# Kernel tuning notes

Measured on AMD Instinct MI355X. Metric: run time of the kernel, lower is better.

The kernel has to match this reference:

```python
import jax, jax.numpy as jnp
import numpy as np

NUM_HEADS = 4
GROUPS = 8
EPS = 1e-5

def setup_inputs() -> dict:
    key = jax.random.key(0)
    ks = jax.random.split(key, 4)
    C = 256
    x = jax.random.normal(ks[0], (4, C, 64, 64), dtype=jnp.float32)
    qkv_w = jax.random.normal(ks[1], (3 * C, C), dtype=jnp.float32) * (C ** -0.5)
    qkv_b = jnp.zeros((3 * C,), dtype=jnp.float32)
    proj_w = jax.random.normal(ks[2], (C, C), dtype=jnp.float32) * (C ** -0.5)
    proj_b = jnp.zeros((C,), dtype=jnp.float32)
    gamma = jnp.ones((C,), dtype=jnp.float32)
    beta = jnp.zeros((C,), dtype=jnp.float32)
    return {"x": x, "qkv_w": qkv_w, "qkv_b": qkv_b, "proj_w": proj_w, "proj_b": proj_b, "gamma": gamma, "beta": beta}

def group_norm(x, gamma, beta):
    B, C, H, W = x.shape
    xg = x.reshape(B, GROUPS, C // GROUPS, H, W)
    mean = xg.mean(axis=(2, 3, 4), keepdims=True)
    var = xg.var(axis=(2, 3, 4), keepdims=True)
    xn = (xg - mean) * jax.lax.rsqrt(var + EPS)
    xn = xn.reshape(B, C, H, W)
    return xn * gamma[None, :, None, None] + beta[None, :, None, None]

def reference(x, qkv_w, qkv_b, proj_w, proj_b, gamma, beta):
    B, C, H, W = x.shape
    L = H * W
    hd = C // NUM_HEADS
    xn = group_norm(x, gamma, beta)  # (B,C,H,W)
    xf = xn.reshape(B, C, L)  # tokens along last axis
    # 1x1 conv == per-pixel linear: (3C, C) @ (B, C, L)
    qkv = jnp.einsum('oc,bcl->bol', qkv_w, xf) + qkv_b[None, :, None]
    q, k, v = jnp.split(qkv, 3, axis=1)  # each (B,C,L)
    q = q.reshape(B, NUM_HEADS, hd, L)
    k = k.reshape(B, NUM_HEADS, hd, L)
    v = v.reshape(B, NUM_HEADS, hd, L)
    scale = hd ** -0.5
    attn = jnp.einsum('bhdq,bhdk->bhqk', q, k) * scale
    attn = jax.nn.softmax(attn, axis=-1)
    out = jnp.einsum('bhqk,bhdk->bhdq', attn, v)  # (B,h,hd,L)
    out = out.reshape(B, C, L)
    out = jnp.einsum('oc,bcl->bol', proj_w, out) + proj_b[None, :, None]
    return out.reshape(B, C, H, W) + xn
```

## Files before the change

kernel.cpp:

```cpp
#include <hip/hip_runtime.h>
#include <math.h>

#define L 4096
#define LOG2E_O8 0.18033688011112042f

typedef float f32x16 __attribute__((ext_vector_type(16)));
typedef __bf16 bf16x8 __attribute__((ext_vector_type(8)));

static __device__ __forceinline__ float fast_exp2(float x) {
    return __builtin_amdgcn_exp2f(x);
}
static __device__ __forceinline__ unsigned short f2bfu(float f) {
    unsigned int u = __builtin_bit_cast(unsigned int, f);
    u += 0x7fffu + ((u >> 16) & 1u);
    return (unsigned short)(u >> 16);
}
static __device__ __forceinline__ unsigned int cvtpk(float a, float b) {
    unsigned int r;
    asm("v_cvt_pk_bf16_f32 %0, %1, %2" : "=v"(r) : "v"(a), "v"(b));
    return r;
}
static __device__ __forceinline__ void pl32swap(unsigned int& a, unsigned int& b) {
    auto r = __builtin_amdgcn_permlane32_swap(a, b, false, false);
    a = r[0];
    b = r[1];
}
static __device__ __forceinline__ bf16x8 ld_frag_g(const unsigned short* p) {
    uint4 v = *(const uint4*)p;
    return __builtin_bit_cast(bf16x8, v);
}
static __device__ __forceinline__ bf16x8 ld_frag_s(const unsigned short* p) {
    uint4 v = *(const uint4*)p;
    return __builtin_bit_cast(bf16x8, v);
}

__global__ __launch_bounds__(256) void gn_stats_part_kernel(const float* __restrict__ x,
                                                            float2* __restrict__ part) {
    const int blk = blockIdx.x;
    const float4* p = (const float4*)(x + (size_t)blk * 8192);
    float sum = 0.f, sq = 0.f;
    for (int i = threadIdx.x; i < 2048; i += 256) {
        float4 v = p[i];
        sum += (v.x + v.y) + (v.z + v.w);
        sq  += (v.x * v.x + v.y * v.y) + (v.z * v.z + v.w * v.w);
    }
#pragma unroll
    for (int off = 1; off < 64; off <<= 1) {
        sum += __shfl_xor(sum, off);
        sq  += __shfl_xor(sq, off);
    }
    __shared__ float red[8];
    const int t = threadIdx.x;
    if ((t & 63) == 0) { red[(t >> 6) * 2] = sum; red[(t >> 6) * 2 + 1] = sq; }
    __syncthreads();
    if (t == 0) {
        float s = red[0] + red[2] + red[4] + red[6];
        float q = red[1] + red[3] + red[5] + red[7];
        part[blk] = make_float2(s, q);
    }
}

__global__ __launch_bounds__(64) void gn_stats_final_kernel(const float2* __restrict__ part,
                                                            float2* __restrict__ stats) {
    const int bg = threadIdx.x;
    if (bg < 32) {
        float s = 0.f, q = 0.f;
#pragma unroll
        for (int i = 0; i < 16; ++i) {
            float2 v = part[bg * 16 + i];
            s += v.x; q += v.y;
        }
        const float inv_n = 1.0f / (32.0f * L);
        float mean = s * inv_n;
        float var = q * inv_n - mean * mean;
        stats[bg] = make_float2(mean, rsqrtf(var + 1e-5f));
    }
}

__global__ __launch_bounds__(256) void wcvt_kernel(const float* __restrict__ qkv_w,
                                                   const float* __restrict__ proj_w,
                                                   unsigned short* __restrict__ Wqb,
                                                   unsigned short* __restrict__ Wpb) {
    const int i4 = (blockIdx.x * 256 + threadIdx.x) * 4;
    const float* src;
    unsigned short* dst;
    if (i4 < 196608) { src = qkv_w + i4; dst = Wqb + i4; }
    else             { src = proj_w + (i4 - 196608); dst = Wpb + (i4 - 196608); }
    float4 v = *(const float4*)src;
    ushort4 o;
    o.x = f2bfu(v.x); o.y = f2bfu(v.y); o.z = f2bfu(v.z); o.w = f2bfu(v.w);
    *(ushort4*)dst = o;
}

__global__ __launch_bounds__(256) void gn_apply_kernel(const float* __restrict__ x,
                                                       const float* __restrict__ gamma,
                                                       const float* __restrict__ beta,
                                                       const float2* __restrict__ stats,
                                                       unsigned short* __restrict__ xnT) {
    __shared__ float tile[64][68];
    const int t = threadIdx.x;
    const int b = blockIdx.z, c0 = blockIdx.y * 64, l0 = blockIdx.x * 64;
    const int lc = (t & 15) * 4, cr = t >> 4;
#pragma unroll
    for (int p = 0; p < 4; ++p) {
        const int c = c0 + cr + p * 16;
        const float2 st = stats[b * 8 + (c >> 5)];
        const float g = gamma[c] * st.y;
        const float be = beta[c] - st.x * g;
        float4 v = *(const float4*)&x[((size_t)b * 256 + c) * L + l0 + lc];
        float4 o;
        o.x = v.x * g + be; o.y = v.y * g + be; o.z = v.z * g + be; o.w = v.w * g + be;
        *(float4*)&tile[cr + p * 16][lc] = o;
    }
    __syncthreads();
    const int lr = t >> 2, cc = (t & 3) * 16;
    unsigned short* dst = &xnT[((size_t)b * L + l0 + lr) * 256 + c0 + cc];
#pragma unroll
    for (int g4 = 0; g4 < 4; ++g4) {
        ushort4 o4;
        o4.x = f2bfu(tile[cc + g4 * 4 + 0][lr]);
        o4.y = f2bfu(tile[cc + g4 * 4 + 1][lr]);
        o4.z = f2bfu(tile[cc + g4 * 4 + 2][lr]);
        o4.w = f2bfu(tile[cc + g4 * 4 + 3][lr]);
        *(ushort4*)&dst[g4 * 4] = o4;
    }
}

__global__ __launch_bounds__(256) void qkv_gemm_kernel(
        const unsigned short* __restrict__ xnT,
        const unsigned short* __restrict__ Wq,
        const float* __restrict__ bias,
        unsigned short* __restrict__ Qb,
        unsigned short* __restrict__ Kb,
        unsigned short* __restrict__ Vb) {
    const int t = threadIdx.x, lane = t & 63, w = t >> 6;
    const int l5 = lane >> 5, l31 = lane & 31;
    const int wn = w & 1, wm = w >> 1;
    const int n0 = blockIdx.x * 128 + wn * 64;
    const int m0 = blockIdx.y * 128 + wm * 64;
    const int b = blockIdx.z;
    const unsigned short* ap = xnT + ((size_t)b * L + n0 + l31) * 256 + l5 * 8;
    const unsigned short* bp = Wq + (size_t)(m0 + l31) * 256 + l5 * 8;
    f32x16 acc[2][2];
#pragma unroll
    for (int i = 0; i < 2; ++i)
#pragma unroll
        for (int j = 0; j < 2; ++j)
#pragma unroll
            for (int r = 0; r < 16; ++r) acc[i][j][r] = 0.f;
#pragma unroll
    for (int k0 = 0; k0 < 256; k0 += 16) {
        bf16x8 a0 = ld_frag_g(ap + k0);
        bf16x8 a1 = ld_frag_g(ap + 32 * 256 + k0);
        bf16x8 b0 = ld_frag_g(bp + k0);
        bf16x8 b1 = ld_frag_g(bp + 32 * 256 + k0);
        acc[0][0] = __builtin_amdgcn_mfma_f32_32x32x16_bf16(a0, b0, acc[0][0], 0, 0, 0);
        acc[0][1] = __builtin_amdgcn_mfma_f32_32x32x16_bf16(a0, b1, acc[0][1], 0, 0, 0);
        acc[1][0] = __builtin_amdgcn_mfma_f32_32x32x16_bf16(a1, b0, acc[1][0], 0, 0, 0);
        acc[1][1] = __builtin_amdgcn_mfma_f32_32x32x16_bf16(a1, b1, acc[1][1], 0, 0, 0);
    }
    const int sec = m0 >> 8;
    const size_t bh = (size_t)(b * 4 + ((m0 >> 6) & 3));
#pragma unroll
    for (int j = 0; j < 2; ++j) {
        const int m = m0 + j * 32 + l31;
        const int d = m & 63;
        const float bi = bias[m];
        if (sec < 2) {
            unsigned short* dst = (sec ? Kb : Qb) + bh * L * 64 + d;
            const float sc = (sec == 0) ? LOG2E_O8 : 1.0f;
#pragma unroll
            for (int i = 0; i < 2; ++i)
#pragma unroll
                for (int r = 0; r < 16; ++r) {
                    const int n = n0 + i * 32 + (r & 3) + 8 * (r >> 2) + 4 * l5;
                    dst[(size_t)n * 64] = f2bfu((acc[i][j][r] + bi) * sc);
                }
        } else {
            unsigned short* dst = Vb + (bh * 64 + d) * L;
#pragma unroll
            for (int i = 0; i < 2; ++i)
#pragma unroll
                for (int g = 0; g < 4; ++g) {
                    const int n = n0 + i * 32 + 8 * g + 4 * l5;
                    ushort4 st;
                    st.x = f2bfu(acc[i][j][4 * g + 0] + bi);
                    st.y = f2bfu(acc[i][j][4 * g + 1] + bi);
                    st.z = f2bfu(acc[i][j][4 * g + 2] + bi);
                    st.w = f2bfu(acc[i][j][4 * g + 3] + bi);
                    *(ushort4*)&dst[n] = st;
                }
        }
    }
}

__global__ __launch_bounds__(256, 2) void attn_kernel(
        const unsigned short* __restrict__ Qb,
        const unsigned short* __restrict__ Kb,
        const unsigned short* __restrict__ Vb,
        unsigned short* __restrict__ aoT) {
    const int t = threadIdx.x;
    const int lane = t & 63, w = t >> 6;
    const int l5 = lane >> 5, l31 = lane & 31;
    const int n = blockIdx.x;
    const int bh_i = n & 15;
    const int qt = n >> 4;
    const int b = bh_i >> 2, h = bh_i & 3;
    const int q0 = qt * 128 + w * 32;
    const size_t bh = (size_t)bh_i;

    __shared__ alignas(16) unsigned short Kt[2][32][72];
    __shared__ alignas(16) unsigned short Vt[2][64][40];

    const unsigned short* qp = Qb + (bh * L + q0 + l31) * 64 + l5 * 8;
    bf16x8 qf[4];
#pragma unroll
    for (int dc = 0; dc < 4; ++dc) qf[dc] = ld_frag_g(qp + dc * 16);

    const int kr = t >> 3, kq = t & 7;
    const int vd = t >> 2, vp = t & 3;
    const unsigned short* kgsrc = Kb + bh * L * 64 + kr * 64 + kq * 8;
    const unsigned short* vgsrc = Vb + (bh * 64 + vd) * L + vp * 8;

    f32x16 o0, o1;
#pragma unroll
    for (int r = 0; r < 16; ++r) { o0[r] = 0.f; o1[r] = 0.f; }
    float4 ls = make_float4(0.f, 0.f, 0.f, 0.f);

    {
        uint4 kv = *(const uint4*)kgsrc;
        uint4 vv = *(const uint4*)vgsrc;
        *(uint4*)&Kt[0][kr][kq * 8] = kv;
        *(uint4*)&Vt[0][vd][vp * 8] = vv;
    }
    __syncthreads();

    for (int kc = 0; kc < 128; ++kc) {
        const int buf = kc & 1;
        uint4 knx, vnx;
        if (kc < 127) {
            knx = *(const uint4*)(kgsrc + (size_t)(kc + 1) * 2048);
            vnx = *(const uint4*)(vgsrc + (kc + 1) * 32);
        }
        bf16x8 kf[4], vf[2][2];
#pragma unroll
        for (int dc = 0; dc < 4; ++dc)
            kf[dc] = ld_frag_s(&Kt[buf][l31][dc * 16 + l5 * 8]);
#pragma unroll
        for (int dh = 0; dh < 2; ++dh)
#pragma unroll
            for (int h16 = 0; h16 < 2; ++h16)
                vf[dh][h16] = ld_frag_s(&Vt[buf][dh * 32 + l31][h16 * 16 + l5 * 8]);
        f32x16 s;
#pragma unroll
        for (int r = 0; r < 16; ++r) s[r] = 0.f;
#pragma unroll
        for (int dc = 0; dc < 4; ++dc)
            s = __builtin_amdgcn_mfma_f32_32x32x16_bf16(kf[dc], qf[dc], s, 0, 0, 0);
#pragma unroll
        for (int r = 0; r < 16; ++r) s[r] = fast_exp2(s[r]);
#pragma unroll
        for (int g = 0; g < 4; ++g) {
            ls.x += s[4 * g + 0];
            ls.y += s[4 * g + 1];
            ls.z += s[4 * g + 2];
            ls.w += s[4 * g + 3];
        }
        unsigned int w0 = cvtpk(s[0],  s[1]);
        unsigned int w1 = cvtpk(s[2],  s[3]);
        unsigned int w2 = cvtpk(s[4],  s[5]);
        unsigned int w3 = cvtpk(s[6],  s[7]);
        unsigned int w4 = cvtpk(s[8],  s[9]);
        unsigned int w5 = cvtpk(s[10], s[11]);
        unsigned int w6 = cvtpk(s[12], s[13]);
        unsigned int w7 = cvtpk(s[14], s[15]);
        pl32swap(w0, w2);
        pl32swap(w1, w3);
        pl32swap(w4, w6);
        pl32swap(w5, w7);
        int4 p0v, p1v;
        p0v.x = (int)w0; p0v.y = (int)w1; p0v.z = (int)w2; p0v.w = (int)w3;
        p1v.x = (int)w4; p1v.y = (int)w5; p1v.z = (int)w6; p1v.w = (int)w7;
        bf16x8 pb0 = __builtin_bit_cast(bf16x8, p0v);
        bf16x8 pb1 = __builtin_bit_cast(bf16x8, p1v);
        o0 = __builtin_amdgcn_mfma_f32_32x32x16_bf16(vf[0][0], pb0, o0, 0, 0, 0);
        o0 = __builtin_amdgcn_mfma_f32_32x32x16_bf16(vf[0][1], pb1, o0, 0, 0, 0);
        o1 = __builtin_amdgcn_mfma_f32_32x32x16_bf16(vf[1][0], pb0, o1, 0, 0, 0);
        o1 = __builtin_amdgcn_mfma_f32_32x32x16_bf16(vf[1][1], pb1, o1, 0, 0, 0);
        if (kc < 127) {
            *(uint4*)&Kt[buf ^ 1][kr][kq * 8] = knx;
            *(uint4*)&Vt[buf ^ 1][vd][vp * 8] = vnx;
        }
        __syncthreads();
    }
    float lrun = (ls.x + ls.y) + (ls.z + ls.w);
    lrun += __shfl_xor(lrun, 32);
    const float inv = 1.f / lrun;
    unsigned short* op = aoT + ((size_t)b * L + q0 + l31) * 256 + h * 64 + 4 * l5;
#pragma unroll
    for (int g = 0; g < 4; ++g) {
        uint2 st;
        st.x = cvtpk(o0[4 * g + 0] * inv, o0[4 * g + 1] * inv);
        st.y = cvtpk(o0[4 * g + 2] * inv, o0[4 * g + 3] * inv);
        *(uint2*)&op[8 * g] = st;
        uint2 st2;
        st2.x = cvtpk(o1[4 * g + 0] * inv, o1[4 * g + 1] * inv);
        st2.y = cvtpk(o1[4 * g + 2] * inv, o1[4 * g + 3] * inv);
        *(uint2*)&op[32 + 8 * g] = st2;
    }
}

__global__ __launch_bounds__(256) void proj_gemm_kernel(
        const unsigned short* __restrict__ aoT,
        const unsigned short* __restrict__ Wp,
        const float* __restrict__ bias,
        const float* __restrict__ x,
        const float* __restrict__ gamma,
        const float* __restrict__ beta,
        const float2* __restrict__ stats,
        float* __restrict__ out) {
    const int t = threadIdx.x, lane = t & 63, w = t >> 6;
    const int l5 = lane >> 5, l31 = lane & 31;
    const int wn = w & 1, wm = w >> 1;
    const int n0 = blockIdx.x * 64 + wn * 32;
    const int m0 = blockIdx.y * 128 + wm * 64;
    const int b = blockIdx.z;
    const unsigned short* ap = aoT + ((size_t)b * L + n0 + l31) * 256 + l5 * 8;
    const unsigned short* bp = Wp + (size_t)(m0 + l31) * 256 + l5 * 8;
    f32x16 acc[2];
#pragma unroll
    for (int j = 0; j < 2; ++j)
#pragma unroll
        for (int r = 0; r < 16; ++r) acc[j][r] = 0.f;
#pragma unroll
    for (int k0 = 0; k0 < 256; k0 += 16) {
        bf16x8 a  = ld_frag_g(ap + k0);
        bf16x8 b0 = ld_frag_g(bp + k0);
        bf16x8 b1 = ld_frag_g(bp + 32 * 256 + k0);
        acc[0] = __builtin_amdgcn_mfma_f32_32x32x16_bf16(a, b0, acc[0], 0, 0, 0);
        acc[1] = __builtin_amdgcn_mfma_f32_32x32x16_bf16(a, b1, acc[1], 0, 0, 0);
    }
#pragma unroll
    for (int j = 0; j < 2; ++j) {
        const int co = m0 + j * 32 + l31;
        const float2 st = stats[b * 8 + (co >> 5)];
        const float g = gamma[co] * st.y;
        const float be = beta[co] - st.x * g + bias[co];
        const float* xr = &x[((size_t)b * 256 + co) * L];
        float* orow = &out[((size_t)b * 256 + co) * L];
#pragma unroll
        for (int q = 0; q < 4; ++q) {
            const int n = n0 + 8 * q + 4 * l5;
            float4 xv = *(const float4*)&xr[n];
            float4 ov;
            ov.x = acc[j][4 * q + 0] + (xv.x * g + be);
            ov.y = acc[j][4 * q + 1] + (xv.y * g + be);
            ov.z = acc[j][4 * q + 2] + (xv.z * g + be);
            ov.w = acc[j][4 * q + 3] + (xv.w * g + be);
            *(float4*)&orow[n] = ov;
        }
    }
}

extern "C" void kernel_launch(void* const* d_in, const int* in_sizes, int n_in,
                              void* d_out, int out_size, void* d_ws, size_t ws_size,
                              hipStream_t stream) {
    const float* x      = (const float*)d_in[0];
    const float* qkv_w  = (const float*)d_in[1];
    const float* qkv_b  = (const float*)d_in[2];
    const float* proj_w = (const float*)d_in[3];
    const float* proj_b = (const float*)d_in[4];
    const float* gamma  = (const float*)d_in[5];
    const float* beta   = (const float*)d_in[6];
    float* out = (float*)d_out;

    char* ws = (char*)d_ws;
    float2* stats       = (float2*)ws;
    unsigned short* Wqb = (unsigned short*)(ws + 512);
    unsigned short* Wpb = (unsigned short*)(ws + 512 + 393216);
    unsigned short* xnT = (unsigned short*)(ws + 524800);
    unsigned short* Qb  = (unsigned short*)(ws + 524800 + 8388608);
    unsigned short* Kb  = Qb + (size_t)16 * L * 64;
    unsigned short* Vb  = Kb + (size_t)16 * L * 64;
    unsigned short* aoT = Vb + (size_t)16 * L * 64;
    float2* spart       = (float2*)(ws + 524800);

    gn_stats_part_kernel<<<dim3(512), dim3(256), 0, stream>>>(x, spart);
    gn_stats_final_kernel<<<dim3(1), dim3(64), 0, stream>>>(spart, stats);
    wcvt_kernel<<<dim3(256), dim3(256), 0, stream>>>(qkv_w, proj_w, Wqb, Wpb);
    gn_apply_kernel<<<dim3(64, 4, 4), dim3(256), 0, stream>>>(x, gamma, beta, stats, xnT);
    qkv_gemm_kernel<<<dim3(32, 6, 4), dim3(256), 0, stream>>>(xnT, Wqb, qkv_b, Qb, Kb, Vb);
    attn_kernel<<<dim3(512), dim3(256), 0, stream>>>(Qb, Kb, Vb, aoT);
    proj_gemm_kernel<<<dim3(64, 2, 4), dim3(256), 0, stream>>>(aoT, Wpb, proj_b, x, gamma, beta, stats, out);
}
```

Baseline: 226.0 us.

## Split attention over key halves and merge partial results in a separate kernel

The attention kernel now splits the 4096-key range into two halves, launching 1024 blocks instead of 512, and writes unnormalized fp32 partial outputs and row sums to workspace. A new merge kernel adds the two partials, normalizes, and writes the bf16 output used by the projection. Launch bounds rise to 4 blocks per CU so more waves can be resident. The cost is about 32 MB of extra fp32 traffic and one more launch. The merge relies on the softmax having no running max, so both halves share the same exponent base.

```diff
diff --git a/kernel.cpp b/kernel.cpp
--- a/kernel.cpp
+++ b/kernel.cpp
@@ -194,18 +194,20 @@
     }
 }
 
-__global__ __launch_bounds__(256, 2) void attn_kernel(
+__global__ __launch_bounds__(256, 4) void attn_kernel(
         const unsigned short* __restrict__ Qb,
         const unsigned short* __restrict__ Kb,
         const unsigned short* __restrict__ Vb,
-        unsigned short* __restrict__ aoT) {
+        float* __restrict__ Po,
+        float* __restrict__ Pl) {
     const int t = threadIdx.x;
     const int lane = t & 63, w = t >> 6;
     const int l5 = lane >> 5, l31 = lane & 31;
     const int n = blockIdx.x;
     const int bh_i = n & 15;
-    const int qt = n >> 4;
-    const int b = bh_i >> 2, h = bh_i & 3;
+    const int r = n >> 4;
+    const int qt = r & 31;
+    const int kh = r >> 5;
     const int q0 = qt * 128 + w * 32;
     const size_t bh = (size_t)bh_i;
 
@@ -219,12 +221,12 @@
 
     const int kr = t >> 3, kq = t & 7;
     const int vd = t >> 2, vp = t & 3;
-    const unsigned short* kgsrc = Kb + bh * L * 64 + kr * 64 + kq * 8;
-    const unsigned short* vgsrc = Vb + (bh * 64 + vd) * L + vp * 8;
+    const unsigned short* kgsrc = Kb + bh * L * 64 + (size_t)kh * 2048 * 64 + kr * 64 + kq * 8;
+    const unsigned short* vgsrc = Vb + (bh * 64 + vd) * L + kh * 2048 + vp * 8;
 
     f32x16 o0, o1;
 #pragma unroll
-    for (int r = 0; r < 16; ++r) { o0[r] = 0.f; o1[r] = 0.f; }
+    for (int r2 = 0; r2 < 16; ++r2) { o0[r2] = 0.f; o1[r2] = 0.f; }
     float4 ls = make_float4(0.f, 0.f, 0.f, 0.f);
 
     {
@@ -235,10 +237,10 @@
     }
     __syncthreads();
 
-    for (int kc = 0; kc < 128; ++kc) {
+    for (int kc = 0; kc < 64; ++kc) {
         const int buf = kc & 1;
         uint4 knx, vnx;
-        if (kc < 127) {
+        if (kc < 63) {
             knx = *(const uint4*)(kgsrc + (size_t)(kc + 1) * 2048);
             vnx = *(const uint4*)(vgsrc + (kc + 1) * 32);
         }
@@ -253,12 +255,12 @@
                 vf[dh][h16] = ld_frag_s(&Vt[buf][dh * 32 + l31][h16 * 16 + l5 * 8]);
         f32x16 s;
 #pragma unroll
-        for (int r = 0; r < 16; ++r) s[r] = 0.f;
+        for (int r2 = 0; r2 < 16; ++r2) s[r2] = 0.f;
 #pragma unroll
         for (int dc = 0; dc < 4; ++dc)
             s = __builtin_amdgcn_mfma_f32_32x32x16_bf16(kf[dc], qf[dc], s, 0, 0, 0);
 #pragma unroll
-        for (int r = 0; r < 16; ++r) s[r] = fast_exp2(s[r]);
+        for (int r2 = 0; r2 < 16; ++r2) s[r2] = fast_exp2(s[r2]);
 #pragma unroll
         for (int g = 0; g < 4; ++g) {
             ls.x += s[4 * g + 0];
@@ -287,7 +289,7 @@
         o0 = __builtin_amdgcn_mfma_f32_32x32x16_bf16(vf[0][1], pb1, o0, 0, 0, 0);
         o1 = __builtin_amdgcn_mfma_f32_32x32x16_bf16(vf[1][0], pb0, o1, 0, 0, 0);
         o1 = __builtin_amdgcn_mfma_f32_32x32x16_bf16(vf[1][1], pb1, o1, 0, 0, 0);
-        if (kc < 127) {
+        if (kc < 63) {
             *(uint4*)&Kt[buf ^ 1][kr][kq * 8] = knx;
             *(uint4*)&Vt[buf ^ 1][vd][vp * 8] = vnx;
         }
@@ -295,18 +297,43 @@
     }
     float lrun = (ls.x + ls.y) + (ls.z + ls.w);
     lrun += __shfl_xor(lrun, 32);
-    const float inv = 1.f / lrun;
-    unsigned short* op = aoT + ((size_t)b * L + q0 + l31) * 256 + h * 64 + 4 * l5;
+    float* pp = Po + ((size_t)(kh * 16 + bh_i) * 4096 + q0 + l31) * 64 + 4 * l5;
 #pragma unroll
     for (int g = 0; g < 4; ++g) {
-        uint2 st;
-        st.x = cvtpk(o0[4 * g + 0] * inv, o0[4 * g + 1] * inv);
-        st.y = cvtpk(o0[4 * g + 2] * inv, o0[4 * g + 3] * inv);
-        *(uint2*)&op[8 * g] = st;
-        uint2 st2;
-        st2.x = cvtpk(o1[4 * g + 0] * inv, o1[4 * g + 1] * inv);
-        st2.y = cvtpk(o1[4 * g + 2] * inv, o1[4 * g + 3] * inv);
-        *(uint2*)&op[32 + 8 * g] = st2;
+        *(float4*)&pp[8 * g] =
+            make_float4(o0[4 * g + 0], o0[4 * g + 1], o0[4 * g + 2], o0[4 * g + 3]);
+        *(float4*)&pp[32 + 8 * g] =
+            make_float4(o1[4 * g + 0], o1[4 * g + 1], o1[4 * g + 2], o1[4 * g + 3]);
+    }
+    if (l5 == 0) Pl[(size_t)(kh * 16 + bh_i) * 4096 + q0 + l31] = lrun;
+}
+
+__global__ __launch_bounds__(256) void attn_merge_kernel(
+        const float* __restrict__ Po,
+        const float* __restrict__ Pl,
+        unsigned short* __restrict__ aoT) {
+    const int t = threadIdx.x;
+    const int ri = blockIdx.x * 64 + (t >> 2);
+    const int d0 = (t & 3) * 16;
+    const int bh = ri >> 12, q = ri & 4095;
+    const int b = bh >> 2, h = bh & 3;
+    const float l0 = Pl[ri], l1 = Pl[65536 + ri];
+    const float inv = 1.f / (l0 + l1);
+    const float* p0 = Po + (size_t)ri * 64 + d0;
+    const float* p1 = p0 + (size_t)65536 * 64;
+    unsigned short* op = aoT + ((size_t)b * L + q) * 256 + h * 64 + d0;
+#pragma unroll
+    for (int g = 0; g < 2; ++g) {
+        float4 a0 = *(const float4*)&p0[g * 8 + 0];
+        float4 a1 = *(const float4*)&p0[g * 8 + 4];
+        float4 c0 = *(const float4*)&p1[g * 8 + 0];
+        float4 c1 = *(const float4*)&p1[g * 8 + 4];
+        uint4 st;
+        st.x = cvtpk((a0.x + c0.x) * inv, (a0.y + c0.y) * inv);
+        st.y = cvtpk((a0.z + c0.z) * inv, (a0.w + c0.w) * inv);
+        st.z = cvtpk((a1.x + c1.x) * inv, (a1.y + c1.y) * inv);
+        st.w = cvtpk((a1.z + c1.z) * inv, (a1.w + c1.w) * inv);
+        *(uint4*)&op[g * 8] = st;
     }
 }
 
@@ -383,6 +410,8 @@
     unsigned short* Kb  = Qb + (size_t)16 * L * 64;
     unsigned short* Vb  = Kb + (size_t)16 * L * 64;
     unsigned short* aoT = Vb + (size_t)16 * L * 64;
+    float* Po           = (float*)(ws + 42467840);
+    float* Pl           = (float*)(ws + 42467840 + 33554432);
     float2* spart       = (float2*)(ws + 524800);
 
     gn_stats_part_kernel<<<dim3(512), dim3(256), 0, stream>>>(x, spart);
@@ -390,6 +419,7 @@
     wcvt_kernel<<<dim3(256), dim3(256), 0, stream>>>(qkv_w, proj_w, Wqb, Wpb);
     gn_apply_kernel<<<dim3(64, 4, 4), dim3(256), 0, stream>>>(x, gamma, beta, stats, xnT);
     qkv_gemm_kernel<<<dim3(32, 6, 4), dim3(256), 0, stream>>>(xnT, Wqb, qkv_b, Qb, Kb, Vb);
-    attn_kernel<<<dim3(512), dim3(256), 0, stream>>>(Qb, Kb, Vb, aoT);
+    attn_kernel<<<dim3(1024), dim3(256), 0, stream>>>(Qb, Kb, Vb, Po, Pl);
+    attn_merge_kernel<<<dim3(1024), dim3(256), 0, stream>>>(Po, Pl, aoT);
     proj_gemm_kernel<<<dim3(64, 2, 4), dim3(256), 0, stream>>>(aoT, Wpb, proj_b, x, gamma, beta, stats, out);
 }
```

New measurement: 221.3 us. 2.1% less time.

## Double key tile per iteration and interleave two S tiles with MFMA priority

Applied to the files above, without the earlier changes.

The attention loop now processes 64 keys per iteration instead of 32, loading two K and V fragment sets and computing two score tiles, which halves the number of barriers and shared-memory staging steps. The exp/convert work of the second tile is interleaved after the first tile's PV MFMAs, and s_setprio raises wave priority around MFMA groups to encourage overlap of matrix and vector work across waves. The launch-bounds occupancy hint of 2 is dropped and shared memory grows, so register pressure and occupancy may change.

```diff
diff --git a/kernel.cpp b/kernel.cpp
--- a/kernel.cpp
+++ b/kernel.cpp
@@ -194,7 +194,7 @@
     }
 }
 
-__global__ __launch_bounds__(256, 2) void attn_kernel(
+__global__ __launch_bounds__(256) void attn_kernel(
         const unsigned short* __restrict__ Qb,
         const unsigned short* __restrict__ Kb,
         const unsigned short* __restrict__ Vb,
@@ -209,87 +209,139 @@
     const int q0 = qt * 128 + w * 32;
     const size_t bh = (size_t)bh_i;
 
-    __shared__ alignas(16) unsigned short Kt[2][32][72];
-    __shared__ alignas(16) unsigned short Vt[2][64][40];
+    __shared__ alignas(16) unsigned short Kt[2][64][72];
+    __shared__ alignas(16) unsigned short Vt[2][64][72];
 
     const unsigned short* qp = Qb + (bh * L + q0 + l31) * 64 + l5 * 8;
     bf16x8 qf[4];
 #pragma unroll
     for (int dc = 0; dc < 4; ++dc) qf[dc] = ld_frag_g(qp + dc * 16);
 
-    const int kr = t >> 3, kq = t & 7;
-    const int vd = t >> 2, vp = t & 3;
-    const unsigned short* kgsrc = Kb + bh * L * 64 + kr * 64 + kq * 8;
-    const unsigned short* vgsrc = Vb + (bh * 64 + vd) * L + vp * 8;
+    const int sr = t >> 2, sp = t & 3;
+    const unsigned short* kgsrc = Kb + bh * L * 64 + sr * 64 + sp * 16;
+    const unsigned short* vgsrc = Vb + (bh * 64 + sr) * L + sp * 16;
 
     f32x16 o0, o1;
 #pragma unroll
-    for (int r = 0; r < 16; ++r) { o0[r] = 0.f; o1[r] = 0.f; }
+    for (int r2 = 0; r2 < 16; ++r2) { o0[r2] = 0.f; o1[r2] = 0.f; }
     float4 ls = make_float4(0.f, 0.f, 0.f, 0.f);
 
     {
-        uint4 kv = *(const uint4*)kgsrc;
-        uint4 vv = *(const uint4*)vgsrc;
-        *(uint4*)&Kt[0][kr][kq * 8] = kv;
-        *(uint4*)&Vt[0][vd][vp * 8] = vv;
+        uint4 k0 = *(const uint4*)kgsrc;
+        uint4 k1 = *(const uint4*)(kgsrc + 8);
+        uint4 v0 = *(const uint4*)vgsrc;
+        uint4 v1 = *(const uint4*)(vgsrc + 8);
+        *(uint4*)&Kt[0][sr][sp * 16]     = k0;
+        *(uint4*)&Kt[0][sr][sp * 16 + 8] = k1;
+        *(uint4*)&Vt[0][sr][sp * 16]     = v0;
+        *(uint4*)&Vt[0][sr][sp * 16 + 8] = v1;
     }
     __syncthreads();
 
-    for (int kc = 0; kc < 128; ++kc) {
-        const int buf = kc & 1;
-        uint4 knx, vnx;
-        if (kc < 127) {
-            knx = *(const uint4*)(kgsrc + (size_t)(kc + 1) * 2048);
-            vnx = *(const uint4*)(vgsrc + (kc + 1) * 32);
-        }
-        bf16x8 kf[4], vf[2][2];
+    for (int ic = 0; ic < 64; ++ic) {
+        const int buf = ic & 1;
+        uint4 kn0, kn1, vn0, vn1;
+        if (ic < 63) {
+            const unsigned short* kg = kgsrc + (size_t)(ic + 1) * 4096;
+            const unsigned short* vg = vgsrc + (ic + 1) * 64;
+            kn0 = *(const uint4*)kg;
+            kn1 = *(const uint4*)(kg + 8);
+            vn0 = *(const uint4*)vg;
+            vn1 = *(const uint4*)(vg + 8);
+        }
+        bf16x8 kf0[4], kf1[4], vf0[2][2], vf1[2][2];
+#pragma unroll
+        for (int dc = 0; dc < 4; ++dc) {
+            kf0[dc] = ld_frag_s(&Kt[buf][l31][dc * 16 + l5 * 8]);
+            kf1[dc] = ld_frag_s(&Kt[buf][32 + l31][dc * 16 + l5 * 8]);
+        }
+#pragma unroll
+        for (int dh = 0; dh < 2; ++dh)
+#pragma unroll
+            for (int h16 = 0; h16 < 2; ++h16) {
+                vf0[dh][h16] = ld_frag_s(&Vt[buf][dh * 32 + l31][h16 * 16 + l5 * 8]);
+                vf1[dh][h16] = ld_frag_s(&Vt[buf][dh * 32 + l31][32 + h16 * 16 + l5 * 8]);
+            }
+        f32x16 s0, s1;
+#pragma unroll
+        for (int r2 = 0; r2 < 16; ++r2) { s0[r2] = 0.f; s1[r2] = 0.f; }
+        __builtin_amdgcn_s_setprio(1);
 #pragma unroll
         for (int dc = 0; dc < 4; ++dc)
-            kf[dc] = ld_frag_s(&Kt[buf][l31][dc * 16 + l5 * 8]);
-#pragma unroll
-        for (int dh = 0; dh < 2; ++dh)
-#pragma unroll
-            for (int h16 = 0; h16 < 2; ++h16)
-                vf[dh][h16] = ld_frag_s(&Vt[buf][dh * 32 + l31][h16 * 16 + l5 * 8]);
-        f32x16 s;
-#pragma unroll
-        for (int r = 0; r < 16; ++r) s[r] = 0.f;
+            s0 = __builtin_amdgcn_mfma_f32_32x32x16_bf16(kf0[dc], qf[dc], s0, 0, 0, 0);
 #pragma unroll
         for (int dc = 0; dc < 4; ++dc)
-            s = __builtin_amdgcn_mfma_f32_32x32x16_bf16(kf[dc], qf[dc], s, 0, 0, 0);
-#pragma unroll
-        for (int r = 0; r < 16; ++r) s[r] = fast_exp2(s[r]);
+            s1 = __builtin_amdgcn_mfma_f32_32x32x16_bf16(kf1[dc], qf[dc], s1, 0, 0, 0);
+        __builtin_amdgcn_s_setprio(0);
+#pragma unroll
+        for (int r2 = 0; r2 < 16; ++r2) s0[r2] = fast_exp2(s0[r2]);
 #pragma unroll
         for (int g = 0; g < 4; ++g) {
-            ls.x += s[4 * g + 0];
-            ls.y += s[4 * g + 1];
-            ls.z += s[4 * g + 2];
-            ls.w += s[4 * g + 3];
-        }
-        unsigned int w0 = cvtpk(s[0],  s[1]);
-        unsigned int w1 = cvtpk(s[2],  s[3]);
-        unsigned int w2 = cvtpk(s[4],  s[5]);
-        unsigned int w3 = cvtpk(s[6],  s[7]);
-        unsigned int w4 = cvtpk(s[8],  s[9]);
-        unsigned int w5 = cvtpk(s[10], s[11]);
-        unsigned int w6 = cvtpk(s[12], s[13]);
-        unsigned int w7 = cvtpk(s[14], s[15]);
-        pl32swap(w0, w2);
-        pl32swap(w1, w3);
-        pl32swap(w4, w6);
-        pl32swap(w5, w7);
-        int4 p0v, p1v;
-        p0v.x = (int)w0; p0v.y = (int)w1; p0v.z = (int)w2; p0v.w = (int)w3;
-        p1v.x = (int)w4; p1v.y = (int)w5; p1v.z = (int)w6; p1v.w = (int)w7;
-        bf16x8 pb0 = __builtin_bit_cast(bf16x8, p0v);
-        bf16x8 pb1 = __builtin_bit_cast(bf16x8, p1v);
-        o0 = __builtin_amdgcn_mfma_f32_32x32x16_bf16(vf[0][0], pb0, o0, 0, 0, 0);
-        o0 = __builtin_amdgcn_mfma_f32_32x32x16_bf16(vf[0][1], pb1, o0, 0, 0, 0);
-        o1 = __builtin_amdgcn_mfma_f32_32x32x16_bf16(vf[1][0], pb0, o1, 0, 0, 0);
-        o1 = __builtin_amdgcn_mfma_f32_32x32x16_bf16(vf[1][1], pb1, o1, 0, 0, 0);
-        if (kc < 127) {
-            *(uint4*)&Kt[buf ^ 1][kr][kq * 8] = knx;
-            *(uint4*)&Vt[buf ^ 1][vd][vp * 8] = vnx;
+            ls.x += s0[4 * g + 0];
+            ls.y += s0[4 * g + 1];
+            ls.z += s0[4 * g + 2];
+            ls.w += s0[4 * g + 3];
+        }
+        unsigned int a0 = cvtpk(s0[0],  s0[1]);
+        unsigned int a1 = cvtpk(s0[2],  s0[3]);
+        unsigned int a2 = cvtpk(s0[4],  s0[5]);
+        unsigned int a3 = cvtpk(s0[6],  s0[7]);
+        unsigned int a4 = cvtpk(s0[8],  s0[9]);
+        unsigned int a5 = cvtpk(s0[10], s0[11]);
+        unsigned int a6 = cvtpk(s0[12], s0[13]);
+        unsigned int a7 = cvtpk(s0[14], s0[15]);
+        pl32swap(a0, a2);
+        pl32swap(a1, a3);
+        pl32swap(a4, a6);
+        pl32swap(a5, a7);
+        int4 pa0, pa1;
+        pa0.x = (int)a0; pa0.y = (int)a1; pa0.z = (int)a2; pa0.w = (int)a3;
+        pa1.x = (int)a4; pa1.y = (int)a5; pa1.z = (int)a6; pa1.w = (int)a7;
+        bf16x8 pb0a = __builtin_bit_cast(bf16x8, pa0);
+        bf16x8 pb1a = __builtin_bit_cast(bf16x8, pa1);
+        __builtin_amdgcn_s_setprio(1);
+        o0 = __builtin_amdgcn_mfma_f32_32x32x16_bf16(vf0[0][0], pb0a, o0, 0, 0, 0);
+        o0 = __builtin_amdgcn_mfma_f32_32x32x16_bf16(vf0[0][1], pb1a, o0, 0, 0, 0);
+        o1 = __builtin_amdgcn_mfma_f32_32x32x16_bf16(vf0[1][0], pb0a, o1, 0, 0, 0);
+        o1 = __builtin_amdgcn_mfma_f32_32x32x16_bf16(vf0[1][1], pb1a, o1, 0, 0, 0);
+        __builtin_amdgcn_s_setprio(0);
+#pragma unroll
+        for (int r2 = 0; r2 < 16; ++r2) s1[r2] = fast_exp2(s1[r2]);
+#pragma unroll
+        for (int g = 0; g < 4; ++g) {
+            ls.x += s1[4 * g + 0];
+            ls.y += s1[4 * g + 1];
+            ls.z += s1[4 * g + 2];
+            ls.w += s1[4 * g + 3];
+        }
+        unsigned int b0 = cvtpk(s1[0],  s1[1]);
+        unsigned int b1 = cvtpk(s1[2],  s1[3]);
+        unsigned int b2 = cvtpk(s1[4],  s1[5]);
+        unsigned int b3 = cvtpk(s1[6],  s1[7]);
+        unsigned int b4 = cvtpk(s1[8],  s1[9]);
+        unsigned int b5 = cvtpk(s1[10], s1[11]);
+        unsigned int b6 = cvtpk(s1[12], s1[13]);
+        unsigned int b7 = cvtpk(s1[14], s1[15]);
+        pl32swap(b0, b2);
+        pl32swap(b1, b3);
+        pl32swap(b4, b6);
+        pl32swap(b5, b7);
+        int4 pb0i, pb1i;
+        pb0i.x = (int)b0; pb0i.y = (int)b1; pb0i.z = (int)b2; pb0i.w = (int)b3;
+        pb1i.x = (int)b4; pb1i.y = (int)b5; pb1i.z = (int)b6; pb1i.w = (int)b7;
+        bf16x8 pb0b = __builtin_bit_cast(bf16x8, pb0i);
+        bf16x8 pb1b = __builtin_bit_cast(bf16x8, pb1i);
+        __builtin_amdgcn_s_setprio(1);
+        o0 = __builtin_amdgcn_mfma_f32_32x32x16_bf16(vf1[0][0], pb0b, o0, 0, 0, 0);
+        o0 = __builtin_amdgcn_mfma_f32_32x32x16_bf16(vf1[0][1], pb1b, o0, 0, 0, 0);
+        o1 = __builtin_amdgcn_mfma_f32_32x32x16_bf16(vf1[1][0], pb0b, o1, 0, 0, 0);
+        o1 = __builtin_amdgcn_mfma_f32_32x32x16_bf16(vf1[1][1], pb1b, o1, 0, 0, 0);
+        __builtin_amdgcn_s_setprio(0);
+        if (ic < 63) {
+            *(uint4*)&Kt[buf ^ 1][sr][sp * 16]     = kn0;
+            *(uint4*)&Kt[buf ^ 1][sr][sp * 16 + 8] = kn1;
+            *(uint4*)&Vt[buf ^ 1][sr][sp * 16]     = vn0;
+            *(uint4*)&Vt[buf ^ 1][sr][sp * 16 + 8] = vn1;
         }
         __syncthreads();
     }
```

New measurement: 230.3 us. Within noise of the previous version (+1.9%).
